# Performance work log

Hardware: AMD Instinct MI355X
Metric: run time of the kernel (lower is better)

The kernel has to match this reference:

```python
import jax, jax.numpy as jnp
import numpy as np

DIM = 512
NUM_HEADS = 8
HEAD_DIM = DIM // NUM_HEADS
SCALE = HEAD_DIM ** -0.5
B, N = 8, 1024


def setup_inputs() -> dict:
    key = jax.random.key(0)
    k1, k2, k3, k4, k5 = jax.random.split(key, 5)
    x = jax.random.normal(k1, (B, N, DIM), dtype=jnp.float32)
    rpe_bias = jax.random.normal(k2, (1, NUM_HEADS, N, N), dtype=jnp.float32)
    # torch Linear weights: [out_features, in_features], y = x @ W.T
    qkv_w = jax.random.normal(k3, (3 * DIM, DIM), dtype=jnp.float32) * (DIM ** -0.5)
    proj_w = jax.random.normal(k4, (DIM, DIM), dtype=jnp.float32) * (DIM ** -0.5)
    proj_b = jax.random.normal(k5, (DIM,), dtype=jnp.float32) * 0.01
    return {"x": x, "rpe_bias": rpe_bias, "qkv_w": qkv_w, "proj_w": proj_w, "proj_b": proj_b}


def reference(x, rpe_bias, qkv_w, proj_w, proj_b):
    b, n, c = x.shape
    h, d = NUM_HEADS, HEAD_DIM
    # qkv projection (no bias): [B,N,3C] -> [3,B,H,N,D]
    qkv = (x @ qkv_w.T).reshape(b, n, 3, h, d).transpose(2, 0, 3, 1, 4)
    q, k, v = qkv[0], qkv[1], qkv[2]
    attn = jnp.einsum('bhnd,bhmd->bhnm', q, k) * SCALE + rpe_bias
    attn = jax.nn.softmax(attn, axis=-1)  # dropout p=0 -> identity
    out = jnp.einsum('bhnm,bhmd->bhnd', attn, v)
    out = out.transpose(0, 2, 1, 3).reshape(b, n, c)
    return out @ proj_w.T + proj_b
```

## Files before the change

kernel.cpp:

```cpp
#include <hip/hip_runtime.h>
#include <hip/hip_bf16.h>

#define B_    8
#define N_    1024
#define DIM_  512
#define H_    8
#define DH_   64
#define SCALE_ 0.125f

typedef unsigned short u16;
typedef __attribute__((ext_vector_type(8))) short bf16x8;
typedef __attribute__((ext_vector_type(4))) short bf16x4;
typedef __attribute__((ext_vector_type(4))) float f32x4;

__device__ __forceinline__ u16 f2bf(float f) {
  union { float f; unsigned u; } v; v.f = f;
  return (u16)((v.u + 0x7fffu + ((v.u >> 16) & 1u)) >> 16);
}
__device__ __forceinline__ unsigned pack2(float a, float b) {
  return (unsigned)f2bf(a) | ((unsigned)f2bf(b) << 16);
}
__device__ __forceinline__ void cp16(const void* g, void* l) {
  __builtin_amdgcn_global_load_lds(
      (const __attribute__((address_space(1))) unsigned*)g,
      (__attribute__((address_space(3))) unsigned*)l, 16, 0, 0);
}

__global__ __launch_bounds__(256) void convert_kernel(
    const float* __restrict__ X, const float* __restrict__ Wq,
    const float* __restrict__ Wp, u16* __restrict__ Xb,
    u16* __restrict__ Wqb, u16* __restrict__ Wpb) {
  const int NX4 = (B_ * N_ * DIM_) / 4;
  const int NQ4 = (3 * DIM_ * DIM_) / 4;
  const int NP4 = (DIM_ * DIM_) / 4;
  const int total = NX4 + NQ4 + NP4;
  const int stride = gridDim.x * 256;
  for (int i = blockIdx.x * 256 + threadIdx.x; i < total; i += stride) {
    const float* s; u16* d; int off;
    if (i < NX4)            { s = X;  d = Xb;  off = i; }
    else if (i < NX4 + NQ4) { s = Wq; d = Wqb; off = i - NX4; }
    else                    { s = Wp; d = Wpb; off = i - NX4 - NQ4; }
    float4 f = *(const float4*)(s + (size_t)off * 4);
    uint2 u; u.x = pack2(f.x, f.y); u.y = pack2(f.z, f.w);
    *(uint2*)(d + (size_t)off * 4) = u;
  }
}

__global__ __launch_bounds__(256, 3) void qkv_gemm(
    const u16* __restrict__ Ab, const u16* __restrict__ Bb,
    u16* __restrict__ Q, u16* __restrict__ K, u16* __restrict__ Vt) {
  __shared__ __align__(16) u16 sA[2][128 * 64];
  __shared__ __align__(16) u16 sB[2][64 * 64];
  const int t = threadIdx.x;
  const int wv = t >> 6, lane = t & 63, quad = (lane >> 4) & 3, l15 = lane & 15;

  const int bid = blockIdx.x;
  const int xcd = bid & 7;
  const int s = bid >> 3;
  const int nti = s >> 3;
  const int m0 = (xcd * 8 + (s & 7)) * 128;
  const int n0 = nti * 64;

  const int srow = lane >> 3;
  const int schunk = (lane & 7) ^ srow;
  const size_t ga = (size_t)(m0 + srow) * DIM_ + schunk * 8;
  const size_t gb = (size_t)(n0 + srow) * DIM_ + schunk * 8;

  f32x4 zero = {0.f, 0.f, 0.f, 0.f};
  f32x4 acc[2][4];
#pragma unroll
  for (int i = 0; i < 2; i++)
#pragma unroll
    for (int j = 0; j < 4; j++) acc[i][j] = zero;

  auto stage = [&](int buf, int k0) {
#pragma unroll
    for (int i = 0; i < 4; i++) {
      const int rb = 32 * wv + 8 * i;
      cp16(Ab + ga + (size_t)rb * DIM_ + k0, &sA[buf][rb * 64]);
    }
#pragma unroll
    for (int i = 0; i < 2; i++) {
      const int rb = 16 * wv + 8 * i;
      cp16(Bb + gb + (size_t)rb * DIM_ + k0, &sB[buf][rb * 64]);
    }
  };

  stage(0, 0);
  for (int kt = 0; kt < 8; kt++) {
    const int cur = kt & 1;
    asm volatile("s_barrier" ::: "memory");
    if (kt < 7) {
      stage(cur ^ 1, (kt + 1) * 64);
      asm volatile("s_waitcnt vmcnt(6)" ::: "memory");
    } else {
      asm volatile("s_waitcnt vmcnt(0)" ::: "memory");
    }
    asm volatile("s_barrier" ::: "memory");
#pragma unroll
    for (int ks = 0; ks < 2; ks++) {
      bf16x8 af[2], bfv[4];
#pragma unroll
      for (int i = 0; i < 2; i++)
        af[i] = *(const bf16x8*)&sA[cur][(wv * 32 + 16 * i + l15) * 64 +
                                        (((ks << 2) | quad) ^ (l15 & 7)) * 8];
#pragma unroll
      for (int j = 0; j < 4; j++)
        bfv[j] = *(const bf16x8*)&sB[cur][(16 * j + l15) * 64 +
                                         (((ks << 2) | quad) ^ (l15 & 7)) * 8];
      __builtin_amdgcn_s_setprio(1);
#pragma unroll
      for (int i = 0; i < 2; i++)
#pragma unroll
        for (int j = 0; j < 4; j++)
          acc[i][j] = __builtin_amdgcn_mfma_f32_16x16x32_bf16(af[i], bfv[j], acc[i][j], 0, 0, 0);
      __builtin_amdgcn_s_setprio(0);
    }
  }

  const int tsel = n0 >> 9;
  const int h = (n0 >> 6) & 7;
#pragma unroll
  for (int j = 0; j < 4; j++) {
    const int jg = n0 + 16 * j + l15;
    const int d = jg & 63;
#pragma unroll
    for (int i = 0; i < 2; i++) {
      const int mbase = m0 + wv * 32 + 16 * i + quad * 4;
      const int b = mbase >> 10, nb = mbase & 1023;
      const size_t bh = (size_t)(b * H_ + h);
      if (tsel == 2) {
        ushort4 v4;
        v4.x = f2bf(acc[i][j][0]); v4.y = f2bf(acc[i][j][1]);
        v4.z = f2bf(acc[i][j][2]); v4.w = f2bf(acc[i][j][3]);
        *(ushort4*)&Vt[(bh * DH_ + d) * N_ + nb] = v4;
      } else {
        u16* dst = (tsel == 0 ? Q : K);
#pragma unroll
        for (int rr = 0; rr < 4; rr++)
          dst[(bh * N_ + nb + rr) * DH_ + d] = f2bf(acc[i][j][rr]);
      }
    }
  }
}

__global__ __launch_bounds__(512, 4) void attn_kernel(
    const u16* __restrict__ Q, const u16* __restrict__ K,
    const u16* __restrict__ Vt, const float* __restrict__ bias,
    u16* __restrict__ AO) {
  __shared__ __align__(16) u16 sK[64 * 64];
  __shared__ __align__(16) u16 sV[64 * 64];
  const int t = threadIdx.x;
  const int wv = t >> 6;
  const int lane = t & 63, quad = (lane >> 4) & 3, l15 = lane & 15;

  const int bid = blockIdx.x;
  const int h = bid & 7;
  const int s = bid >> 3;
  const int nx = s >> 3;
  const int b = s & 7;
  const int n0 = nx << 7;
  const int bh = b * H_ + h;

  const int qg = n0 + 16 * wv + l15;
  bf16x8 qf0, qf1;
  {
    const u16* qa = Q + (((size_t)bh << 10) + qg) * DH_ + (quad << 3);
    qf0 = *(const bf16x8*)qa; qf1 = *(const bf16x8*)(qa + 32);
  }

  const float* bp = bias + (((size_t)h << 10) + qg) * N_ + (quad << 2);

  const int r = t >> 3, c8 = t & 7;
  const u16* kbase = K + (((size_t)bh << 10) + r) * DH_ + (c8 << 3);
  const u16* vbase = Vt + (((size_t)bh << 6) + r) * N_ + (c8 << 3);
  const int so = r * 128 + ((c8 ^ (r & 7)) << 4);

  const int rx = (l15 & 7) << 4;
  const int frow = l15 * 128;
  const int vhalf = (quad & 1) << 3;

  f32x4 zero = {0.f, 0.f, 0.f, 0.f};
  f32x4 O[4];
  O[0] = zero; O[1] = zero; O[2] = zero; O[3] = zero;
  float lsum = 0.f;

  uint4 kr = *(const uint4*)kbase;
  uint4 vr = *(const uint4*)vbase;

  for (int kt = 0; kt < 16; kt++) {
    __syncthreads();
    *(uint4*)((char*)sK + so) = kr;
    *(uint4*)((char*)sV + so) = vr;
    if (kt < 15) {
      kr = *(const uint4*)(kbase + (size_t)(kt + 1) * 64 * DH_);
      vr = *(const uint4*)(vbase + (kt + 1) * 64);
    }
    float4 b4[4];
#pragma unroll
    for (int cb = 0; cb < 4; cb++)
      b4[cb] = *(const float4*)(bp + (kt << 6) + 16 * cb);
    __syncthreads();

    bf16x8 kf[8];
#pragma unroll
    for (int ks = 0; ks < 2; ks++)
#pragma unroll
      for (int cb = 0; cb < 4; cb++)
        kf[ks * 4 + cb] = *(const bf16x8*)((const char*)sK + cb * 2048 + frow +
                                           (((ks << 6) | (quad << 4)) ^ rx));

    f32x4 S[4];
    S[0] = zero; S[1] = zero; S[2] = zero; S[3] = zero;
    __builtin_amdgcn_s_setprio(1);
#pragma unroll
    for (int ks = 0; ks < 2; ks++) {
      const bf16x8 qf = ks ? qf1 : qf0;
#pragma unroll
      for (int cb = 0; cb < 4; cb++)
        S[cb] = __builtin_amdgcn_mfma_f32_16x16x32_bf16(kf[ks * 4 + cb], qf, S[cb], 0, 0, 0);
    }
    __builtin_amdgcn_s_setprio(0);

    bf16x4 p[4];
#pragma unroll
    for (int cb = 0; cb < 4; cb++) {
      float p0 = __expf(fmaf(S[cb][0], SCALE_, b4[cb].x));
      float p1 = __expf(fmaf(S[cb][1], SCALE_, b4[cb].y));
      float p2 = __expf(fmaf(S[cb][2], SCALE_, b4[cb].z));
      float p3 = __expf(fmaf(S[cb][3], SCALE_, b4[cb].w));
      lsum += (p0 + p1) + (p2 + p3);
      uint2 pk; pk.x = pack2(p0, p1); pk.y = pack2(p2, p3);
      p[cb] = __builtin_bit_cast(bf16x4, pk);
    }

    __builtin_amdgcn_s_setprio(1);
#pragma unroll
    for (int cbp = 0; cbp < 4; cbp++) {
      bf16x4 vf[4];
#pragma unroll
      for (int cb = 0; cb < 4; cb++) {
        const int ch = ((((2 * cb + (quad >> 1)) << 4)) ^ rx) + vhalf;
        vf[cb] = *(const bf16x4*)((const char*)sV + cbp * 2048 + frow + ch);
      }
#pragma unroll
      for (int cb = 0; cb < 4; cb++)
        O[cbp] = __builtin_amdgcn_mfma_f32_16x16x16bf16_1k(vf[cb], p[cb], O[cbp], 0, 0, 0);
    }
    __builtin_amdgcn_s_setprio(0);
  }

  lsum += __shfl_xor(lsum, 16);
  lsum += __shfl_xor(lsum, 32);
  const float inv = 1.f / lsum;
#pragma unroll
  for (int cb = 0; cb < 4; cb++) {
    ushort4 o4;
    o4.x = f2bf(O[cb][0] * inv); o4.y = f2bf(O[cb][1] * inv);
    o4.z = f2bf(O[cb][2] * inv); o4.w = f2bf(O[cb][3] * inv);
    *(ushort4*)&AO[(((size_t)b << 10) + qg) * DIM_ + h * DH_ + 16 * cb + (quad << 2)] = o4;
  }
}

__global__ __launch_bounds__(256, 3) void proj_gemm(
    const u16* __restrict__ Ab, const u16* __restrict__ Bb,
    const float* __restrict__ Pb, float* __restrict__ Out) {
  __shared__ __align__(16) u16 sA[2][128 * 64];
  __shared__ __align__(16) u16 sB[2][64 * 64];
  const int t = threadIdx.x;
  const int wv = t >> 6, lane = t & 63, quad = (lane >> 4) & 3, l15 = lane & 15;

  const int bid = blockIdx.x;
  const int xcd = bid & 7;
  const int s = bid >> 3;
  const int nti = s >> 3;
  const int m0 = (xcd * 8 + (s & 7)) * 128;
  const int n0 = nti * 64;

  const int srow = lane >> 3;
  const int schunk = (lane & 7) ^ srow;
  const size_t ga = (size_t)(m0 + srow) * DIM_ + schunk * 8;
  const size_t gb = (size_t)(n0 + srow) * DIM_ + schunk * 8;

  f32x4 zero = {0.f, 0.f, 0.f, 0.f};
  f32x4 acc[2][4];
#pragma unroll
  for (int i = 0; i < 2; i++)
#pragma unroll
    for (int j = 0; j < 4; j++) acc[i][j] = zero;

  auto stage = [&](int buf, int k0) {
#pragma unroll
    for (int i = 0; i < 4; i++) {
      const int rb = 32 * wv + 8 * i;
      cp16(Ab + ga + (size_t)rb * DIM_ + k0, &sA[buf][rb * 64]);
    }
#pragma unroll
    for (int i = 0; i < 2; i++) {
      const int rb = 16 * wv + 8 * i;
      cp16(Bb + gb + (size_t)rb * DIM_ + k0, &sB[buf][rb * 64]);
    }
  };

  stage(0, 0);
  for (int kt = 0; kt < 8; kt++) {
    const int cur = kt & 1;
    asm volatile("s_barrier" ::: "memory");
    if (kt < 7) {
      stage(cur ^ 1, (kt + 1) * 64);
      asm volatile("s_waitcnt vmcnt(6)" ::: "memory");
    } else {
      asm volatile("s_waitcnt vmcnt(0)" ::: "memory");
    }
    asm volatile("s_barrier" ::: "memory");
#pragma unroll
    for (int ks = 0; ks < 2; ks++) {
      bf16x8 af[2], bfv[4];
#pragma unroll
      for (int i = 0; i < 2; i++)
        af[i] = *(const bf16x8*)&sA[cur][(wv * 32 + 16 * i + l15) * 64 +
                                        (((ks << 2) | quad) ^ (l15 & 7)) * 8];
#pragma unroll
      for (int j = 0; j < 4; j++)
        bfv[j] = *(const bf16x8*)&sB[cur][(16 * j + l15) * 64 +
                                         (((ks << 2) | quad) ^ (l15 & 7)) * 8];
      __builtin_amdgcn_s_setprio(1);
#pragma unroll
      for (int i = 0; i < 2; i++)
#pragma unroll
        for (int j = 0; j < 4; j++)
          acc[i][j] = __builtin_amdgcn_mfma_f32_16x16x32_bf16(af[i], bfv[j], acc[i][j], 0, 0, 0);
      __builtin_amdgcn_s_setprio(0);
    }
  }

#pragma unroll
  for (int j = 0; j < 4; j++) {
    const int jg = n0 + 16 * j + l15;
    const float pb = Pb[jg];
#pragma unroll
    for (int i = 0; i < 2; i++) {
      const int mbase = m0 + wv * 32 + 16 * i + quad * 4;
#pragma unroll
      for (int rr = 0; rr < 4; rr++)
        Out[(size_t)(mbase + rr) * DIM_ + jg] = acc[i][j][rr] + pb;
    }
  }
}

extern "C" void kernel_launch(void* const* d_in, const int* in_sizes, int n_in,
                              void* d_out, int out_size, void* d_ws, size_t ws_size,
                              hipStream_t stream) {
  const float* x      = (const float*)d_in[0];
  const float* rpe    = (const float*)d_in[1];
  const float* qkv_w  = (const float*)d_in[2];
  const float* proj_w = (const float*)d_in[3];
  const float* proj_b = (const float*)d_in[4];
  float* out = (float*)d_out;

  const size_t perbuf = (size_t)B_ * N_ * DIM_;
  u16* Xb  = (u16*)d_ws;
  u16* Q   = Xb + perbuf;
  u16* K   = Q + perbuf;
  u16* Vt  = K + perbuf;
  u16* Wqb = Vt + perbuf;
  u16* Wpb = Wqb + (size_t)3 * DIM_ * DIM_;
  u16* AO  = Xb;

  convert_kernel<<<2560, 256, 0, stream>>>(x, qkv_w, proj_w, Xb, Wqb, Wpb);
  qkv_gemm<<<1536, 256, 0, stream>>>(Xb, Wqb, Q, K, Vt);
  attn_kernel<<<512, 512, 0, stream>>>(Q, K, Vt, rpe, AO);
  proj_gemm<<<512, 256, 0, stream>>>(AO, Wpb, proj_b, out);
}
```

Measured before the change: 162.7 us.

## Double-buffer K/V tiles via direct global-to-LDS loads and prefetch bias

Replaces the register-staged K/V tile loads with global_load_lds async copies into double-buffered shared memory, so the next tile streams in while the current one is computed. The source column is pre-swizzled so the direct LDS write keeps the XOR layout. The bias for the next tile is now prefetched one iteration ahead, in the middle of compute. Synchronisation moves to hand-written s_waitcnt/s_barrier sequences with fixed vmcnt counts, which depend on exact instruction ordering and double LDS use per block.

Result: slower. 167.1 us (+2.7%).

```diff
diff --git a/kernel.cpp b/kernel.cpp
--- a/kernel.cpp
+++ b/kernel.cpp
@@ -148,8 +148,8 @@
     const u16* __restrict__ Q, const u16* __restrict__ K,
     const u16* __restrict__ Vt, const float* __restrict__ bias,
     u16* __restrict__ AO) {
-  __shared__ __align__(16) u16 sK[64 * 64];
-  __shared__ __align__(16) u16 sV[64 * 64];
+  __shared__ __align__(16) u16 sK[2][64 * 64];
+  __shared__ __align__(16) u16 sV[2][64 * 64];
   const int t = threadIdx.x;
   const int wv = t >> 6;
   const int lane = t & 63, quad = (lane >> 4) & 3, l15 = lane & 15;
@@ -172,9 +172,10 @@
   const float* bp = bias + (((size_t)h << 10) + qg) * N_ + (quad << 2);
 
   const int r = t >> 3, c8 = t & 7;
-  const u16* kbase = K + (((size_t)bh << 10) + r) * DH_ + (c8 << 3);
-  const u16* vbase = Vt + (((size_t)bh << 6) + r) * N_ + (c8 << 3);
-  const int so = r * 128 + ((c8 ^ (r & 7)) << 4);
+  const int sc = (c8 ^ (r & 7)) << 3;
+  const u16* kbase = K + (((size_t)bh << 10) + r) * DH_ + sc;
+  const u16* vbase = Vt + (((size_t)bh << 6) + r) * N_ + sc;
+  const int wb = wv * 512;
 
   const int rx = (l15 & 7) << 4;
   const int frow = l15 * 128;
@@ -185,29 +186,31 @@
   O[0] = zero; O[1] = zero; O[2] = zero; O[3] = zero;
   float lsum = 0.f;
 
-  uint4 kr = *(const uint4*)kbase;
-  uint4 vr = *(const uint4*)vbase;
+  cp16(kbase, &sK[0][wb]);
+  cp16(vbase, &sV[0][wb]);
+  asm volatile("" ::: "memory");
+  float4 b4[4];
+#pragma unroll
+  for (int cb = 0; cb < 4; cb++) b4[cb] = *(const float4*)(bp + 16 * cb);
 
   for (int kt = 0; kt < 16; kt++) {
-    __syncthreads();
-    *(uint4*)((char*)sK + so) = kr;
-    *(uint4*)((char*)sV + so) = vr;
+    const int cur = kt & 1;
+    asm volatile("s_waitcnt lgkmcnt(0)\n\ts_barrier" ::: "memory");
     if (kt < 15) {
-      kr = *(const uint4*)(kbase + (size_t)(kt + 1) * 64 * DH_);
-      vr = *(const uint4*)(vbase + (kt + 1) * 64);
-    }
-    float4 b4[4];
-#pragma unroll
-    for (int cb = 0; cb < 4; cb++)
-      b4[cb] = *(const float4*)(bp + (kt << 6) + 16 * cb);
-    __syncthreads();
+      cp16(kbase + (size_t)(kt + 1) * 64 * DH_, &sK[cur ^ 1][wb]);
+      cp16(vbase + (kt + 1) * 64, &sV[cur ^ 1][wb]);
+      asm volatile("s_waitcnt vmcnt(6)" ::: "memory");
+    } else {
+      asm volatile("s_waitcnt vmcnt(4)" ::: "memory");
+    }
+    asm volatile("s_barrier" ::: "memory");
 
     bf16x8 kf[8];
 #pragma unroll
     for (int ks = 0; ks < 2; ks++)
 #pragma unroll
       for (int cb = 0; cb < 4; cb++)
-        kf[ks * 4 + cb] = *(const bf16x8*)((const char*)sK + cb * 2048 + frow +
+        kf[ks * 4 + cb] = *(const bf16x8*)((const char*)sK[cur] + cb * 2048 + frow +
                                            (((ks << 6) | (quad << 4)) ^ rx));
 
     f32x4 S[4];
@@ -233,6 +236,11 @@
       uint2 pk; pk.x = pack2(p0, p1); pk.y = pack2(p2, p3);
       p[cb] = __builtin_bit_cast(bf16x4, pk);
     }
+    if (kt < 15) {
+#pragma unroll
+      for (int cb = 0; cb < 4; cb++)
+        b4[cb] = *(const float4*)(bp + ((kt + 1) << 6) + 16 * cb);
+    }
 
     __builtin_amdgcn_s_setprio(1);
 #pragma unroll
@@ -241,7 +249,7 @@
 #pragma unroll
       for (int cb = 0; cb < 4; cb++) {
         const int ch = ((((2 * cb + (quad >> 1)) << 4)) ^ rx) + vhalf;
-        vf[cb] = *(const bf16x4*)((const char*)sV + cbp * 2048 + frow + ch);
+        vf[cb] = *(const bf16x4*)((const char*)sV[cur] + cbp * 2048 + frow + ch);
       }
 #pragma unroll
       for (int cb = 0; cb < 4; cb++)
```

## Split attention KV loop across wave halves with LDS merge and async loads

Applied to the files above, without the earlier changes.

The attention kernel now gives each block 64 queries instead of 128 and launches twice as many blocks. The two halves of the 8 waves each process alternate KV tiles and merge partial outputs and row sums through LDS at the end. K/V tiles are now loaded directly into LDS with global_load_lds instead of register staging, and the launch bound asks for more occupancy. This is meant to raise parallelism and hide load latency, at the cost of an extra LDS reduction and reloading Q and K/V per block.

Result: slower. 282.0 us (+73.3%).

```diff
diff --git a/kernel.cpp b/kernel.cpp
--- a/kernel.cpp
+++ b/kernel.cpp
@@ -144,25 +144,26 @@
   }
 }
 
-__global__ __launch_bounds__(512, 4) void attn_kernel(
+__global__ __launch_bounds__(512, 8) void attn_kernel(
     const u16* __restrict__ Q, const u16* __restrict__ K,
     const u16* __restrict__ Vt, const float* __restrict__ bias,
     u16* __restrict__ AO) {
-  __shared__ __align__(16) u16 sK[64 * 64];
-  __shared__ __align__(16) u16 sV[64 * 64];
+  __shared__ __align__(16) u16 sKV[2][2][64 * 64];
   const int t = threadIdx.x;
   const int wv = t >> 6;
   const int lane = t & 63, quad = (lane >> 4) & 3, l15 = lane & 15;
+  const int hf = wv >> 2;
+  const int wl = wv & 3;
 
   const int bid = blockIdx.x;
   const int h = bid & 7;
   const int s = bid >> 3;
   const int nx = s >> 3;
   const int b = s & 7;
-  const int n0 = nx << 7;
+  const int n0 = nx << 6;
   const int bh = b * H_ + h;
 
-  const int qg = n0 + 16 * wv + l15;
+  const int qg = n0 + 16 * wl + l15;
   bf16x8 qf0, qf1;
   {
     const u16* qa = Q + (((size_t)bh << 10) + qg) * DH_ + (quad << 3);
@@ -171,31 +172,35 @@
 
   const float* bp = bias + (((size_t)h << 10) + qg) * N_ + (quad << 2);
 
-  const int r = t >> 3, c8 = t & 7;
-  const u16* kbase = K + (((size_t)bh << 10) + r) * DH_ + (c8 << 3);
-  const u16* vbase = Vt + (((size_t)bh << 6) + r) * N_ + (c8 << 3);
-  const int so = r * 128 + ((c8 ^ (r & 7)) << 4);
+  const int rr1 = wl * 8 + (lane >> 3);
+  const int sc = ((lane & 7) ^ (lane >> 3)) << 3;
+  const u16* kSrc1 = K + (((size_t)bh << 10) + rr1) * DH_ + sc;
+  const u16* kSrc2 = K + (((size_t)bh << 10) + rr1 + 32) * DH_ + sc;
+  const u16* vSrc1 = Vt + (((size_t)bh << 6) + rr1) * N_ + sc;
+  const u16* vSrc2 = Vt + (((size_t)bh << 6) + rr1 + 32) * N_ + sc;
+  u16* dK1 = &sKV[0][hf][wl * 512];
+  u16* dK2 = &sKV[0][hf][2048 + wl * 512];
+  u16* dV1 = &sKV[1][hf][wl * 512];
+  u16* dV2 = &sKV[1][hf][2048 + wl * 512];
 
   const int rx = (l15 & 7) << 4;
   const int frow = l15 * 128;
   const int vhalf = (quad & 1) << 3;
+  const char* cK = (const char*)&sKV[0][hf][0];
+  const char* cV = (const char*)&sKV[1][hf][0];
 
   f32x4 zero = {0.f, 0.f, 0.f, 0.f};
   f32x4 O[4];
   O[0] = zero; O[1] = zero; O[2] = zero; O[3] = zero;
   float lsum = 0.f;
 
-  uint4 kr = *(const uint4*)kbase;
-  uint4 vr = *(const uint4*)vbase;
-
-  for (int kt = 0; kt < 16; kt++) {
+  for (int pt = 0; pt < 8; pt++) {
+    const int kt = 2 * pt + hf;
     __syncthreads();
-    *(uint4*)((char*)sK + so) = kr;
-    *(uint4*)((char*)sV + so) = vr;
-    if (kt < 15) {
-      kr = *(const uint4*)(kbase + (size_t)(kt + 1) * 64 * DH_);
-      vr = *(const uint4*)(vbase + (kt + 1) * 64);
-    }
+    cp16(kSrc1 + (size_t)kt * 64 * DH_, dK1);
+    cp16(kSrc2 + (size_t)kt * 64 * DH_, dK2);
+    cp16(vSrc1 + kt * 64, dV1);
+    cp16(vSrc2 + kt * 64, dV2);
     float4 b4[4];
 #pragma unroll
     for (int cb = 0; cb < 4; cb++)
@@ -207,7 +212,7 @@
     for (int ks = 0; ks < 2; ks++)
 #pragma unroll
       for (int cb = 0; cb < 4; cb++)
-        kf[ks * 4 + cb] = *(const bf16x8*)((const char*)sK + cb * 2048 + frow +
+        kf[ks * 4 + cb] = *(const bf16x8*)(cK + cb * 2048 + frow +
                                            (((ks << 6) | (quad << 4)) ^ rx));
 
     f32x4 S[4];
@@ -241,7 +246,7 @@
 #pragma unroll
       for (int cb = 0; cb < 4; cb++) {
         const int ch = ((((2 * cb + (quad >> 1)) << 4)) ^ rx) + vhalf;
-        vf[cb] = *(const bf16x4*)((const char*)sV + cbp * 2048 + frow + ch);
+        vf[cb] = *(const bf16x4*)(cV + cbp * 2048 + frow + ch);
       }
 #pragma unroll
       for (int cb = 0; cb < 4; cb++)
@@ -252,13 +257,29 @@
 
   lsum += __shfl_xor(lsum, 16);
   lsum += __shfl_xor(lsum, 32);
-  const float inv = 1.f / lsum;
-#pragma unroll
-  for (int cb = 0; cb < 4; cb++) {
-    ushort4 o4;
-    o4.x = f2bf(O[cb][0] * inv); o4.y = f2bf(O[cb][1] * inv);
-    o4.z = f2bf(O[cb][2] * inv); o4.w = f2bf(O[cb][3] * inv);
-    *(ushort4*)&AO[(((size_t)b << 10) + qg) * DIM_ + h * DH_ + 16 * cb + (quad << 2)] = o4;
+
+  __syncthreads();
+  float* mg = (float*)sKV;
+  if (wv >= 4) {
+    float* d = mg + ((size_t)((wv - 4) * 64 + lane)) * 20;
+#pragma unroll
+    for (int cb = 0; cb < 4; cb++) *(f32x4*)(d + 4 * cb) = O[cb];
+    d[16] = lsum;
+  }
+  __syncthreads();
+  if (wv < 4) {
+    const float* d2 = mg + (size_t)(wv * 64 + lane) * 20;
+#pragma unroll
+    for (int cb = 0; cb < 4; cb++) O[cb] += *(const f32x4*)(d2 + 4 * cb);
+    lsum += d2[16];
+    const float inv = 1.f / lsum;
+#pragma unroll
+    for (int cb = 0; cb < 4; cb++) {
+      ushort4 o4;
+      o4.x = f2bf(O[cb][0] * inv); o4.y = f2bf(O[cb][1] * inv);
+      o4.z = f2bf(O[cb][2] * inv); o4.w = f2bf(O[cb][3] * inv);
+      *(ushort4*)&AO[(((size_t)b << 10) + qg) * DIM_ + h * DH_ + 16 * cb + (quad << 2)] = o4;
+    }
   }
 }
 
@@ -369,6 +390,6 @@
 
   convert_kernel<<<2560, 256, 0, stream>>>(x, qkv_w, proj_w, Xb, Wqb, Wpb);
   qkv_gemm<<<1536, 256, 0, stream>>>(Xb, Wqb, Q, K, Vt);
-  attn_kernel<<<512, 512, 0, stream>>>(Q, K, Vt, rpe, AO);
+  attn_kernel<<<1024, 512, 0, stream>>>(Q, K, Vt, rpe, AO);
   proj_gemm<<<512, 256, 0, stream>>>(AO, Wpb, proj_b, out);
 }
```
